# Optimization experiments

Measured on AMD Instinct MI355X. Metric: run time of the kernel, lower is better.

The kernel has to match this reference:

```python
import jax, jax.numpy as jnp
import numpy as np

RADIUS = 7
EPS = 0.01
K = 2 * RADIUS + 1  # 15x15 box kernel
# TF tf.image.rgb_to_grayscale luma weights
RGB_W = np.array([0.2989, 0.5870, 0.1140], dtype=np.float32)


def setup_inputs() -> dict:
    key = jax.random.key(0)
    # images in [-1, 1], NHWC
    x = jax.random.uniform(key, (16, 512, 512, 3), jnp.float32, -1.0, 1.0)
    return {"x": x}


def reference(x):
    inputs = (x + 1.0) * 0.5  # map to [0, 1]
    # grayscale guidance: [B, H, W, 1]
    guidance = jnp.einsum('bhwc,c->bhw', inputs, jnp.asarray(RGB_W, dtype=x.dtype))[..., None]
    guidance = guidance - jnp.mean(guidance) + jnp.mean(inputs)
    # 15x15 uniform box blur (depthwise conv on the single guidance channel), SAME zero padding
    kernel = jnp.full((K, K, 1, 1), 1.0 / (K * K), dtype=x.dtype)  # HWIO
    smoothed = jax.lax.conv_general_dilated(
        guidance, kernel, window_strides=(1, 1), padding='SAME',
        dimension_numbers=('NHWC', 'HWIO', 'NHWC'))
    out = inputs * (1.0 - EPS) + smoothed * EPS  # smoothed broadcasts over 3 channels
    return out * 2.0 - 1.0
```

## Files before the change

kernel.cpp:

```cpp
#include <hip/hip_runtime.h>


#define BATCH  16
#define HEIGHT 512
#define WIDTH  512
#define NPIX   (BATCH * HEIGHT * WIDTH)
#define RAD    7
#define KS     15
#define EPSV   0.01f

#define W_R 0.2989f
#define W_G 0.5870f
#define W_B 0.1140f
#define WSUM (W_R + W_G + W_B)

typedef _Float16 h4 __attribute__((ext_vector_type(4)));

__global__ __launch_bounds__(256) void k_luma_hblur(const float* __restrict__ x,
                                                    h4* __restrict__ tmp,
                                                    float2* __restrict__ partials) {
    __shared__ float sl[2][528];
    __shared__ float redG[4], redI[4];
    int t  = threadIdx.x;
    int lr = t >> 7;
    int tc = t & 127;
    int c0 = tc << 2;

    if (t < 8) {
        sl[0][t] = 0.f; sl[1][t] = 0.f;
        sl[0][520 + t] = 0.f; sl[1][520 + t] = 0.f;
    }

    const float4* xv = (const float4*)x;
    size_t tb = (size_t)blockIdx.x * 768 + 3 * t;
    float4 A = xv[tb + 0];
    float4 B = xv[tb + 1];
    float4 C = xv[tb + 2];

    float d0 = W_R * A.x + W_G * A.y + W_B * A.z;
    float d1 = W_R * A.w + W_G * B.x + W_B * B.y;
    float d2 = W_R * B.z + W_G * B.w + W_B * C.x;
    float d3 = W_R * C.y + W_G * C.z + W_B * C.w;
    float l0 = 0.5f * d0 + (0.5f * WSUM);
    float l1 = 0.5f * d1 + (0.5f * WSUM);
    float l2 = 0.5f * d2 + (0.5f * WSUM);
    float l3 = 0.5f * d3 + (0.5f * WSUM);

    *(float4*)&sl[lr][8 + c0] = make_float4(l0, l1, l2, l3);

    float sG = (l0 + l1) + (l2 + l3);
    float sx = ((A.x + A.y) + (A.z + A.w))
             + ((B.x + B.y) + (B.z + B.w))
             + ((C.x + C.y) + (C.z + C.w));
    float sI = 0.5f * sx + 6.0f;
#pragma unroll
    for (int off = 32; off > 0; off >>= 1) {
        sG += __shfl_down(sG, off, 64);
        sI += __shfl_down(sI, off, 64);
    }
    int lane = t & 63, wave = t >> 6;
    if (lane == 0) { redG[wave] = sG; redI[wave] = sI; }
    __syncthreads();

    if (t == 0)
        partials[blockIdx.x] = make_float2(redG[0] + redG[1] + redG[2] + redG[3],
                                           redI[0] + redI[1] + redI[2] + redI[3]);

    const float4* rowv = (const float4*)&sl[lr][c0];
    float4 p0 = rowv[0];
    float4 p1 = rowv[1];
    float4 p2 = rowv[2];
    float4 p3 = rowv[3];
    float4 p4 = rowv[4];

    float s1_3   = (p0.y + p0.z) + p0.w;
    float s4_7   = (p1.x + p1.y) + (p1.z + p1.w);
    float s8_11  = (p2.x + p2.y) + (p2.z + p2.w);
    float s12_15 = (p3.x + p3.y) + (p3.z + p3.w);
    float o0 = (s1_3 + s4_7) + (s8_11 + s12_15);
    float o1 = o0 + p4.x - p0.y;
    float o2 = o1 + p4.y - p0.z;
    float o3 = o2 + p4.z - p0.w;

    h4 hv; hv.x = (_Float16)o0; hv.y = (_Float16)o1; hv.z = (_Float16)o2; hv.w = (_Float16)o3;
    tmp[(size_t)(blockIdx.x * 2 + lr) * 128 + tc] = hv;
}

#define TROWS 8
__global__ __launch_bounds__(256) void k_vblur_combine(const h4* __restrict__ tmp,
                                                       const float* __restrict__ x,
                                                       float* __restrict__ out,
                                                       const float2* __restrict__ partials) {
    __shared__ float rr[8];
    int t = threadIdx.x;

    float sG = 0.f, sI = 0.f;
#pragma unroll
    for (int i = 0; i < 16; i++) {
        float2 v = partials[t + (i << 8)];
        sG += v.x; sI += v.y;
    }
#pragma unroll
    for (int off = 32; off > 0; off >>= 1) {
        sG += __shfl_down(sG, off, 64);
        sI += __shfl_down(sI, off, 64);
    }
    int lane = t & 63, wave = t >> 6;
    if (lane == 0) { rr[wave] = sG; rr[4 + wave] = sI; }
    __syncthreads();
    float offset = (rr[4] + rr[5] + rr[6] + rr[7]) * (1.f / (3.f * (float)NPIX))
                 - (rr[0] + rr[1] + rr[2] + rr[3]) * (1.f / (float)NPIX);

    int half = t >> 7;
    int tc   = t & 127;
    int band = blockIdx.x & 31;
    int b    = blockIdx.x >> 5;
    int y0   = band * 16 + half * TROWS;
    const float nrm   = 1.f / (float)(KS * KS);
    const float scale = 1.f - EPSV;

    int col = tc << 2;
    float c0 = (float)(min(col + 0, RAD) + 1 + min(WIDTH - 1 - col, RAD));
    float c1 = (float)(min(col + 1, RAD) + 1 + min(WIDTH - 2 - col, RAD));
    float c2 = (float)(min(col + 2, RAD) + 1 + min(WIDTH - 3 - col, RAD));
    float c3 = (float)(min(col + 3, RAD) + 1 + min(WIDTH - 4 - col, RAD));

    const h4* tv = tmp + (size_t)b * HEIGHT * 128 + tc;

    float s0 = 0.f, s1 = 0.f, s2 = 0.f, s3 = 0.f;
    int rlo = y0 - RAD < 0 ? 0 : y0 - RAD;
    for (int r = rlo; r <= y0 + RAD; ++r) {
        h4 v = tv[(size_t)r * 128];
        s0 += (float)v.x; s1 += (float)v.y; s2 += (float)v.z; s3 += (float)v.w;
    }

    const float4* xv = (const float4*)x + (size_t)b * HEIGHT * 384;
    float4*       ov = (float4*)out     + (size_t)b * HEIGHT * 384;

#pragma unroll
    for (int i = 0; i < TROWS; ++i) {
        int y = y0 + i;
        float cy = (float)(min(y, RAD) + 1 + min(HEIGHT - 1 - y, RAD));
        float k  = offset * cy;
        float a0 = EPSV * (2.f * (s0 + k * c0) * nrm - 1.f);
        float a1 = EPSV * (2.f * (s1 + k * c1) * nrm - 1.f);
        float a2 = EPSV * (2.f * (s2 + k * c2) * nrm - 1.f);
        float a3 = EPSV * (2.f * (s3 + k * c3) * nrm - 1.f);

        size_t rb = (size_t)y * 384 + 3 * tc;
        float4 x0 = xv[rb + 0];
        float4 x1 = xv[rb + 1];
        float4 x2 = xv[rb + 2];
        float4 o0, o1, o2;
        o0.x = x0.x * scale + a0; o0.y = x0.y * scale + a0;
        o0.z = x0.z * scale + a0; o0.w = x0.w * scale + a1;
        o1.x = x1.x * scale + a1; o1.y = x1.y * scale + a1;
        o1.z = x1.z * scale + a2; o1.w = x1.w * scale + a2;
        o2.x = x2.x * scale + a2; o2.y = x2.y * scale + a3;
        o2.z = x2.z * scale + a3; o2.w = x2.w * scale + a3;
        ov[rb + 0] = o0;
        ov[rb + 1] = o1;
        ov[rb + 2] = o2;

        if (y + RAD + 1 < HEIGHT) {
            h4 v = tv[(size_t)(y + RAD + 1) * 128];
            s0 += (float)v.x; s1 += (float)v.y; s2 += (float)v.z; s3 += (float)v.w;
        }
        if (y - RAD >= 0) {
            h4 v = tv[(size_t)(y - RAD) * 128];
            s0 -= (float)v.x; s1 -= (float)v.y; s2 -= (float)v.z; s3 -= (float)v.w;
        }
    }
}

extern "C" void kernel_launch(void* const* d_in, const int* in_sizes, int n_in,
                              void* d_out, int out_size, void* d_ws, size_t ws_size,
                              hipStream_t stream) {
    const float* x   = (const float*)d_in[0];
    float*       out = (float*)d_out;

    float2* partials = (float2*)d_ws;
    h4*     tmp      = (h4*)((char*)d_ws + 32768);

    k_luma_hblur<<<BATCH * HEIGHT / 2, 256, 0, stream>>>(x, tmp, partials);
    k_vblur_combine<<<BATCH * (HEIGHT / 16), 256, 0, stream>>>(tmp, x, out, partials);
}
```

Before: 111.1 us.

## Fuse luma/hblur and vblur/combine into one cooperative kernel with LDS-cached input

Merges the two passes into a single cooperative-launch kernel of 512 blocks, each owning a 16-row band. The band's input is kept in LDS as fp16 so the combine phase does not read x from global memory a second time. A grid-wide sync replaces the kernel boundary for the global-mean reduction, and the old two-kernel path stays as a fallback if the cooperative launch fails. In exchange, each block loops over rows with a barrier per pass, uses about 57 KB of LDS (which limits blocks per CU), and storing x in fp16 adds rounding error to the output.

Measured after the change: 168.1 us. +51.2%, slower.

```diff
diff --git a/kernel.cpp b/kernel.cpp
--- a/kernel.cpp
+++ b/kernel.cpp
@@ -1,4 +1,7 @@
 #include <hip/hip_runtime.h>
+#include <hip/hip_cooperative_groups.h>
+
+namespace cg = cooperative_groups;
 
 
 #define BATCH  16
@@ -15,6 +18,172 @@
 #define WSUM (W_R + W_G + W_B)
 
 typedef _Float16 h4 __attribute__((ext_vector_type(4)));
+
+__global__ __launch_bounds__(256) void k_fused(const float* __restrict__ x,
+                                               float* __restrict__ out,
+                                               h4* __restrict__ tmp,
+                                               float2* __restrict__ partials) {
+    __shared__ h4    xh[16][384];
+    __shared__ float sl[2][2][528];
+    __shared__ float red[8];
+
+    int t  = threadIdx.x;
+    int lr = t >> 7;
+    int tc = t & 127;
+    int c0 = tc << 2;
+
+    int bid  = blockIdx.x;
+    int lb   = (bid & 7) * 64 + (bid >> 3);
+    int bimg = lb >> 5;
+    int band = lb & 31;
+    int y0   = band << 4;
+
+    const float4* xv = (const float4*)x + (size_t)bimg * (512 * 384);
+    h4*           tg = tmp               + (size_t)bimg * (512 * 128);
+
+    if (t < 8) {
+        sl[0][0][t] = 0.f; sl[0][1][t] = 0.f; sl[1][0][t] = 0.f; sl[1][1][t] = 0.f;
+        sl[0][0][520 + t] = 0.f; sl[0][1][520 + t] = 0.f;
+        sl[1][0][520 + t] = 0.f; sl[1][1][520 + t] = 0.f;
+    }
+
+    float sG = 0.f, sI = 0.f;
+#pragma unroll
+    for (int p = 0; p < 8; ++p) {
+        int row = (p << 1) | lr;
+        size_t tb = (size_t)(y0 + (p << 1)) * 384 + 3 * t;
+        float4 A = xv[tb + 0];
+        float4 B = xv[tb + 1];
+        float4 C = xv[tb + 2];
+
+        float d0 = W_R * A.x + W_G * A.y + W_B * A.z;
+        float d1 = W_R * A.w + W_G * B.x + W_B * B.y;
+        float d2 = W_R * B.z + W_G * B.w + W_B * C.x;
+        float d3 = W_R * C.y + W_G * C.z + W_B * C.w;
+        float l0 = 0.5f * d0 + (0.5f * WSUM);
+        float l1 = 0.5f * d1 + (0.5f * WSUM);
+        float l2 = 0.5f * d2 + (0.5f * WSUM);
+        float l3 = 0.5f * d3 + (0.5f * WSUM);
+
+        float* slp = sl[p & 1][lr];
+        *(float4*)&slp[8 + c0] = make_float4(l0, l1, l2, l3);
+
+        h4 xa, xb, xc;
+        xa.x = (_Float16)A.x; xa.y = (_Float16)A.y; xa.z = (_Float16)A.z; xa.w = (_Float16)A.w;
+        xb.x = (_Float16)B.x; xb.y = (_Float16)B.y; xb.z = (_Float16)B.z; xb.w = (_Float16)B.w;
+        xc.x = (_Float16)C.x; xc.y = (_Float16)C.y; xc.z = (_Float16)C.z; xc.w = (_Float16)C.w;
+        xh[row][3 * tc + 0] = xa;
+        xh[row][3 * tc + 1] = xb;
+        xh[row][3 * tc + 2] = xc;
+
+        sG += (l0 + l1) + (l2 + l3);
+        float sx = ((A.x + A.y) + (A.z + A.w))
+                 + ((B.x + B.y) + (B.z + B.w))
+                 + ((C.x + C.y) + (C.z + C.w));
+        sI += 0.5f * sx + 6.0f;
+
+        __syncthreads();
+
+        const float4* rowv = (const float4*)&slp[c0];
+        float4 q0 = rowv[0], q1 = rowv[1], q2 = rowv[2], q3 = rowv[3], q4 = rowv[4];
+        float s1_3   = (q0.y + q0.z) + q0.w;
+        float s4_7   = (q1.x + q1.y) + (q1.z + q1.w);
+        float s8_11  = (q2.x + q2.y) + (q2.z + q2.w);
+        float s12_15 = (q3.x + q3.y) + (q3.z + q3.w);
+        float o0 = (s1_3 + s4_7) + (s8_11 + s12_15);
+        float o1 = o0 + q4.x - q0.y;
+        float o2 = o1 + q4.y - q0.z;
+        float o3 = o2 + q4.z - q0.w;
+
+        h4 hv; hv.x = (_Float16)o0; hv.y = (_Float16)o1; hv.z = (_Float16)o2; hv.w = (_Float16)o3;
+        tg[(size_t)(y0 + row) * 128 + tc] = hv;
+    }
+
+#pragma unroll
+    for (int off = 32; off > 0; off >>= 1) {
+        sG += __shfl_down(sG, off, 64);
+        sI += __shfl_down(sI, off, 64);
+    }
+    if ((t & 63) == 0) { red[t >> 6] = sG; red[4 + (t >> 6)] = sI; }
+    __syncthreads();
+    if (t == 0)
+        partials[bid] = make_float2(red[0] + red[1] + red[2] + red[3],
+                                    red[4] + red[5] + red[6] + red[7]);
+
+    cg::this_grid().sync();
+
+    float2 v0 = partials[t], v1 = partials[t + 256];
+    float pG = v0.x + v1.x, pI = v0.y + v1.y;
+#pragma unroll
+    for (int off = 32; off > 0; off >>= 1) {
+        pG += __shfl_down(pG, off, 64);
+        pI += __shfl_down(pI, off, 64);
+    }
+    if ((t & 63) == 0) { red[t >> 6] = pG; red[4 + (t >> 6)] = pI; }
+    __syncthreads();
+    float offset = (red[4] + red[5] + red[6] + red[7]) * (1.f / (3.f * (float)NPIX))
+                 - (red[0] + red[1] + red[2] + red[3]) * (1.f / (float)NPIX);
+
+    int half = t >> 7;
+    int ys0  = y0 + half * 8;
+    const float nrm   = 1.f / (float)(KS * KS);
+    const float scale = 1.f - EPSV;
+
+    int col = tc << 2;
+    float cc0 = (float)(min(col + 0, RAD) + 1 + min(WIDTH - 1 - col, RAD));
+    float cc1 = (float)(min(col + 1, RAD) + 1 + min(WIDTH - 2 - col, RAD));
+    float cc2 = (float)(min(col + 2, RAD) + 1 + min(WIDTH - 3 - col, RAD));
+    float cc3 = (float)(min(col + 3, RAD) + 1 + min(WIDTH - 4 - col, RAD));
+
+    const h4* tv = tg + tc;
+
+    float s0 = 0.f, s1 = 0.f, s2 = 0.f, s3 = 0.f;
+    int rlo = ys0 - RAD < 0 ? 0 : ys0 - RAD;
+    for (int r = rlo; r <= ys0 + RAD; ++r) {
+        h4 v = tv[(size_t)r * 128];
+        s0 += (float)v.x; s1 += (float)v.y; s2 += (float)v.z; s3 += (float)v.w;
+    }
+
+    float4* ov = (float4*)out + (size_t)bimg * (512 * 384);
+
+#pragma unroll
+    for (int i = 0; i < 8; ++i) {
+        int y   = ys0 + i;
+        int row = (half << 3) + i;
+        float cy = (float)(min(y, RAD) + 1 + min(HEIGHT - 1 - y, RAD));
+        float k  = offset * cy;
+        float a0 = EPSV * (2.f * (s0 + k * cc0) * nrm - 1.f);
+        float a1 = EPSV * (2.f * (s1 + k * cc1) * nrm - 1.f);
+        float a2 = EPSV * (2.f * (s2 + k * cc2) * nrm - 1.f);
+        float a3 = EPSV * (2.f * (s3 + k * cc3) * nrm - 1.f);
+
+        h4 xa = xh[row][3 * tc + 0];
+        h4 xb = xh[row][3 * tc + 1];
+        h4 xc = xh[row][3 * tc + 2];
+
+        float4 o0, o1, o2;
+        o0.x = (float)xa.x * scale + a0; o0.y = (float)xa.y * scale + a0;
+        o0.z = (float)xa.z * scale + a0; o0.w = (float)xa.w * scale + a1;
+        o1.x = (float)xb.x * scale + a1; o1.y = (float)xb.y * scale + a1;
+        o1.z = (float)xb.z * scale + a2; o1.w = (float)xb.w * scale + a2;
+        o2.x = (float)xc.x * scale + a2; o2.y = (float)xc.y * scale + a3;
+        o2.z = (float)xc.z * scale + a3; o2.w = (float)xc.w * scale + a3;
+
+        size_t rb = (size_t)y * 384 + 3 * tc;
+        ov[rb + 0] = o0;
+        ov[rb + 1] = o1;
+        ov[rb + 2] = o2;
+
+        if (y + RAD + 1 < HEIGHT) {
+            h4 v = tv[(size_t)(y + RAD + 1) * 128];
+            s0 += (float)v.x; s1 += (float)v.y; s2 += (float)v.z; s3 += (float)v.w;
+        }
+        if (y - RAD >= 0) {
+            h4 v = tv[(size_t)(y - RAD) * 128];
+            s0 -= (float)v.x; s1 -= (float)v.y; s2 -= (float)v.z; s3 -= (float)v.w;
+        }
+    }
+}
 
 __global__ __launch_bounds__(256) void k_luma_hblur(const float* __restrict__ x,
                                                     h4* __restrict__ tmp,
@@ -182,6 +351,11 @@
     float2* partials = (float2*)d_ws;
     h4*     tmp      = (h4*)((char*)d_ws + 32768);
 
-    k_luma_hblur<<<BATCH * HEIGHT / 2, 256, 0, stream>>>(x, tmp, partials);
-    k_vblur_combine<<<BATCH * (HEIGHT / 16), 256, 0, stream>>>(tmp, x, out, partials);
+    void* args[] = { (void*)&x, (void*)&out, (void*)&tmp, (void*)&partials };
+    hipError_t e = hipLaunchCooperativeKernel((const void*)k_fused, dim3(512), dim3(256),
+                                              args, 0, stream);
+    if (e != hipSuccess) {
+        k_luma_hblur<<<BATCH * HEIGHT / 2, 256, 0, stream>>>(x, tmp, partials);
+        k_vblur_combine<<<BATCH * (HEIGHT / 16), 256, 0, stream>>>(tmp, x, out, partials);
+    }
 }
```
